# Optimization experiments

Measured on AMD Instinct MI355X. Metric: run time of the kernel, lower is better.

The kernel has to match this reference:

```python
import jax, jax.numpy as jnp
import numpy as np
import itertools

FIXED = (128, 128, 128)
NUM_STEPS = 7


def _trilinear(vol, coords):
    """Trilinear sample of vol (D,H,W,C) at voxel-space coords (D,H,W,3),
    with coordinates clamped to the volume boundary (DeepReg resample behavior)."""
    D, H, W, _ = vol.shape
    max_f = jnp.asarray([D - 1, H - 1, W - 1], dtype=coords.dtype)
    max_i = jnp.asarray([D - 1, H - 1, W - 1], dtype=jnp.int32)
    c = jnp.clip(coords, 0.0, max_f)
    c0 = jnp.floor(c)
    w = c - c0                      # fractional weights in [0,1)
    i0 = c0.astype(jnp.int32)
    i1 = jnp.minimum(i0 + 1, max_i)
    out = jnp.zeros_like(vol)
    for b0, b1, b2 in itertools.product((0, 1), repeat=3):
        ii = i1[..., 0] if b0 else i0[..., 0]
        jj = i1[..., 1] if b1 else i0[..., 1]
        kk = i1[..., 2] if b2 else i0[..., 2]
        wt = ((w[..., 0] if b0 else 1.0 - w[..., 0])
              * (w[..., 1] if b1 else 1.0 - w[..., 1])
              * (w[..., 2] if b2 else 1.0 - w[..., 2]))
        out = out + vol[ii, jj, kk] * wt[..., None]
    return out


_warp = jax.vmap(_trilinear)  # over batch: vol (B,D,H,W,C), coords (B,D,H,W,3)


def setup_inputs() -> dict:
    key = jax.random.key(0)
    dvf = jax.random.normal(key, (2, *FIXED, 3), dtype=jnp.float32)
    return {"dvf": dvf}


def reference(dvf):
    D, H, W = FIXED
    grid = jnp.stack(
        jnp.meshgrid(jnp.arange(D), jnp.arange(H), jnp.arange(W), indexing="ij"),
        axis=-1,
    ).astype(dvf.dtype)                      # (D,H,W,3) reference grid
    ddf = dvf / (2.0 ** NUM_STEPS)
    for _ in range(NUM_STEPS):               # scaling-and-squaring
        ddf = ddf + _warp(ddf, grid[None] + ddf)
    return ddf
```

## Files before the change

### kernel.cpp

```cpp
#include <hip/hip_runtime.h>


#define M_   (1 << 21)
#define NVOX (1 << 22)

typedef _Float16 h4 __attribute__((ext_vector_type(4)));
typedef _Float16 h8 __attribute__((ext_vector_type(8)));
struct __attribute__((packed, aligned(8))) H8U { h8 v; };

__global__ __launch_bounds__(256) void t_kernel(const float* __restrict__ src,
                                                h4* __restrict__ dst) {
    const int t = blockIdx.x * blockDim.x + threadIdx.x;
    const float s = 1.0f / 128.0f;
    const float4* s4 = (const float4*)src;
    const float4 a = s4[3 * t + 0];
    const float4 b = s4[3 * t + 1];
    const float4 c = s4[3 * t + 2];
    h4 o0 = { (_Float16)(a.x * s), (_Float16)(a.y * s), (_Float16)(a.z * s), (_Float16)0.f };
    h4 o1 = { (_Float16)(a.w * s), (_Float16)(b.x * s), (_Float16)(b.y * s), (_Float16)0.f };
    h4 o2 = { (_Float16)(b.z * s), (_Float16)(b.w * s), (_Float16)(c.x * s), (_Float16)0.f };
    h4 o3 = { (_Float16)(c.y * s), (_Float16)(c.z * s), (_Float16)(c.w * s), (_Float16)0.f };
    dst[4 * t + 0] = o0;
    dst[4 * t + 1] = o1;
    dst[4 * t + 2] = o2;
    dst[4 * t + 3] = o3;
}

template <bool AOS_OUT>
__global__ __launch_bounds__(256) void step_k(const h4* __restrict__ src,
                                              h4* __restrict__ dst,
                                              float* __restrict__ daos) {
    const int idx = blockIdx.x * blockDim.x + threadIdx.x;
    const int x = idx & 127;
    const int y = (idx >> 7) & 127;
    const int z = (idx >> 14) & 127;
    const int bb = idx & M_;

    const h4 c = src[idx];
    const float v0 = (float)c[0];
    const float v1 = (float)c[1];
    const float v2 = (float)c[2];

    const float cz = fminf(fmaxf((float)z + v0, 0.0f), 127.0f);
    const float cy = fminf(fmaxf((float)y + v1, 0.0f), 127.0f);
    const float cx = fminf(fmaxf((float)x + v2, 0.0f), 127.0f);

    const float fz = floorf(cz), fy = floorf(cy), fx = floorf(cx);
    const float wz = cz - fz, wy = cy - fy, wx = cx - fx;
    const int i0z = (int)fz, i0y = (int)fy, i0x = (int)fx;
    const int i1z = min(i0z + 1, 127);
    const int i1y = min(i0y + 1, 127);
    const float wz0 = 1.0f - wz, wy0 = 1.0f - wy, wx0 = 1.0f - wx;

    float o0 = 0.0f, o1 = 0.0f, o2 = 0.0f;
    #pragma unroll
    for (int b0 = 0; b0 < 2; ++b0) {
        const int   iz  = (b0 ? i1z : i0z) << 14;
        const float wwz = b0 ? wz : wz0;
        #pragma unroll
        for (int b1 = 0; b1 < 2; ++b1) {
            const int   iy  = (b1 ? i1y : i0y) << 7;
            const float w01 = wwz * (b1 ? wy : wy0);
            const H8U* p = (const H8U*)(src + (bb + (iz | iy) + i0x));
            const h8 q = p->v;
            const float wa = w01 * wx0, wb = w01 * wx;
            o0 += wa * (float)q[0] + wb * (float)q[4];
            o1 += wa * (float)q[1] + wb * (float)q[5];
            o2 += wa * (float)q[2] + wb * (float)q[6];
        }
    }

    const float r0 = v0 + o0, r1 = v1 + o1, r2 = v2 + o2;
    if (AOS_OUT) {
        float* d = daos + (size_t)idx * 3;
        d[0] = r0; d[1] = r1; d[2] = r2;
    } else {
        h4 r = { (_Float16)r0, (_Float16)r1, (_Float16)r2, (_Float16)0.f };
        dst[idx] = r;
    }
}

extern "C" void kernel_launch(void* const* d_in, const int* in_sizes, int n_in,
                              void* d_out, int out_size, void* d_ws, size_t ws_size,
                              hipStream_t stream) {
    const float* dvf = (const float*)d_in[0];
    float* out = (float*)d_out;

    h4* B = (h4*)d_ws;
    h4* A = (h4*)d_out;

    const dim3 blk(256);
    const dim3 grd(NVOX / 256);
    const dim3 grd4(NVOX / 4 / 256);

    t_kernel<<<grd4, blk, 0, stream>>>(dvf, B);
    step_k<false><<<grd, blk, 0, stream>>>(B, A, nullptr);
    step_k<false><<<grd, blk, 0, stream>>>(A, B, nullptr);
    step_k<false><<<grd, blk, 0, stream>>>(B, A, nullptr);
    step_k<false><<<grd, blk, 0, stream>>>(A, B, nullptr);
    step_k<false><<<grd, blk, 0, stream>>>(B, A, nullptr);
    step_k<false><<<grd, blk, 0, stream>>>(A, B, nullptr);
    step_k<true> <<<grd, blk, 0, stream>>>(B, nullptr, out);
}
```

Measured before the change: 177.1 us.

## Fuse fp32-to-fp16 conversion into first step and swizzle block-to-XCD mapping

Removes the separate conversion kernel. The first squaring step now reads the fp32 AoS input directly, scaling it by 1/128 and gathering neighbours from fp32. All steps also remap block indices so each group of eight consecutive launched blocks is spread across contiguous volume slabs, aiming for better L2 locality per XCD on MI355X. The first step's fp32 gathers are wider and unaligned, which may cost more than the removed kernel saved.

```diff
diff --git a/kernel.cpp b/kernel.cpp
--- a/kernel.cpp
+++ b/kernel.cpp
@@ -3,43 +3,38 @@
 
 #define M_   (1 << 21)
 #define NVOX (1 << 22)
+#define NBLK (NVOX / 256)
 
 typedef _Float16 h4 __attribute__((ext_vector_type(4)));
 typedef _Float16 h8 __attribute__((ext_vector_type(8)));
 struct __attribute__((packed, aligned(8))) H8U { h8 v; };
 
-__global__ __launch_bounds__(256) void t_kernel(const float* __restrict__ src,
-                                                h4* __restrict__ dst) {
-    const int t = blockIdx.x * blockDim.x + threadIdx.x;
-    const float s = 1.0f / 128.0f;
-    const float4* s4 = (const float4*)src;
-    const float4 a = s4[3 * t + 0];
-    const float4 b = s4[3 * t + 1];
-    const float4 c = s4[3 * t + 2];
-    h4 o0 = { (_Float16)(a.x * s), (_Float16)(a.y * s), (_Float16)(a.z * s), (_Float16)0.f };
-    h4 o1 = { (_Float16)(a.w * s), (_Float16)(b.x * s), (_Float16)(b.y * s), (_Float16)0.f };
-    h4 o2 = { (_Float16)(b.z * s), (_Float16)(b.w * s), (_Float16)(c.x * s), (_Float16)0.f };
-    h4 o3 = { (_Float16)(c.y * s), (_Float16)(c.z * s), (_Float16)(c.w * s), (_Float16)0.f };
-    dst[4 * t + 0] = o0;
-    dst[4 * t + 1] = o1;
-    dst[4 * t + 2] = o2;
-    dst[4 * t + 3] = o3;
+__device__ __forceinline__ int swz_voxel() {
+    const int wb = ((blockIdx.x & 7) * (NBLK / 8)) + (blockIdx.x >> 3);
+    return wb * 256 + threadIdx.x;
 }
 
-template <bool AOS_OUT>
-__global__ __launch_bounds__(256) void step_k(const h4* __restrict__ src,
+template <int MODE>
+__global__ __launch_bounds__(256) void step_k(const float* __restrict__ srcf,
+                                              const h4* __restrict__ src,
                                               h4* __restrict__ dst,
                                               float* __restrict__ daos) {
-    const int idx = blockIdx.x * blockDim.x + threadIdx.x;
+    const int idx = swz_voxel();
     const int x = idx & 127;
     const int y = (idx >> 7) & 127;
     const int z = (idx >> 14) & 127;
     const int bb = idx & M_;
 
-    const h4 c = src[idx];
-    const float v0 = (float)c[0];
-    const float v1 = (float)c[1];
-    const float v2 = (float)c[2];
+    const float scale = (MODE == 0) ? (1.0f / 128.0f) : 1.0f;
+
+    float v0, v1, v2;
+    if (MODE == 0) {
+        const float* p = srcf + (size_t)idx * 3;
+        v0 = p[0] * scale; v1 = p[1] * scale; v2 = p[2] * scale;
+    } else {
+        const h4 c = src[idx];
+        v0 = (float)c[0]; v1 = (float)c[1]; v2 = (float)c[2];
+    }
 
     const float cz = fminf(fmaxf((float)z + v0, 0.0f), 127.0f);
     const float cy = fminf(fmaxf((float)y + v1, 0.0f), 127.0f);
@@ -61,17 +56,27 @@
         for (int b1 = 0; b1 < 2; ++b1) {
             const int   iy  = (b1 ? i1y : i0y) << 7;
             const float w01 = wwz * (b1 ? wy : wy0);
-            const H8U* p = (const H8U*)(src + (bb + (iz | iy) + i0x));
-            const h8 q = p->v;
-            const float wa = w01 * wx0, wb = w01 * wx;
-            o0 += wa * (float)q[0] + wb * (float)q[4];
-            o1 += wa * (float)q[1] + wb * (float)q[5];
-            o2 += wa * (float)q[2] + wb * (float)q[6];
+            if (MODE == 0) {
+                const int i1x = min(i0x + 1, 127);
+                const float* qa = srcf + (size_t)(bb + (iz | iy) + i0x) * 3;
+                const float* qb = srcf + (size_t)(bb + (iz | iy) + i1x) * 3;
+                const float wa = w01 * wx0, wb = w01 * wx;
+                o0 += wa * qa[0] + wb * qb[0];
+                o1 += wa * qa[1] + wb * qb[1];
+                o2 += wa * qa[2] + wb * qb[2];
+            } else {
+                const H8U* p = (const H8U*)(src + (bb + (iz | iy) + i0x));
+                const h8 q = p->v;
+                const float wa = w01 * wx0, wb = w01 * wx;
+                o0 += wa * (float)q[0] + wb * (float)q[4];
+                o1 += wa * (float)q[1] + wb * (float)q[5];
+                o2 += wa * (float)q[2] + wb * (float)q[6];
+            }
         }
     }
 
-    const float r0 = v0 + o0, r1 = v1 + o1, r2 = v2 + o2;
-    if (AOS_OUT) {
+    const float r0 = v0 + o0 * scale, r1 = v1 + o1 * scale, r2 = v2 + o2 * scale;
+    if (MODE == 2) {
         float* d = daos + (size_t)idx * 3;
         d[0] = r0; d[1] = r1; d[2] = r2;
     } else {
@@ -86,19 +91,17 @@
     const float* dvf = (const float*)d_in[0];
     float* out = (float*)d_out;
 
+    h4* A = (h4*)d_out;
     h4* B = (h4*)d_ws;
-    h4* A = (h4*)d_out;
 
     const dim3 blk(256);
-    const dim3 grd(NVOX / 256);
-    const dim3 grd4(NVOX / 4 / 256);
+    const dim3 grd(NBLK);
 
-    t_kernel<<<grd4, blk, 0, stream>>>(dvf, B);
-    step_k<false><<<grd, blk, 0, stream>>>(B, A, nullptr);
-    step_k<false><<<grd, blk, 0, stream>>>(A, B, nullptr);
-    step_k<false><<<grd, blk, 0, stream>>>(B, A, nullptr);
-    step_k<false><<<grd, blk, 0, stream>>>(A, B, nullptr);
-    step_k<false><<<grd, blk, 0, stream>>>(B, A, nullptr);
-    step_k<false><<<grd, blk, 0, stream>>>(A, B, nullptr);
-    step_k<true> <<<grd, blk, 0, stream>>>(B, nullptr, out);
+    step_k<0><<<grd, blk, 0, stream>>>(dvf, nullptr, A, nullptr);
+    step_k<1><<<grd, blk, 0, stream>>>(nullptr, A, B, nullptr);
+    step_k<1><<<grd, blk, 0, stream>>>(nullptr, B, A, nullptr);
+    step_k<1><<<grd, blk, 0, stream>>>(nullptr, A, B, nullptr);
+    step_k<1><<<grd, blk, 0, stream>>>(nullptr, B, A, nullptr);
+    step_k<1><<<grd, blk, 0, stream>>>(nullptr, A, B, nullptr);
+    step_k<2><<<grd, blk, 0, stream>>>(nullptr, B, nullptr, out);
 }
```

After: 167.5 us. -5.4%, faster.
